# Kernel tuning notes

Hardware: AMD Instinct MI355X
Metric: run time of the kernel (lower is better)

## Reference

```python
import jax, jax.numpy as jnp
import numpy as np

N_VEH, N_PED = 16, 16
DV, DP = 40, 24            # vehicle / pedestrian slot obs dims
N = N_VEH + N_PED          # 32 agents
E, H = 128, 4              # embed_dim, num_heads
DH = E // H                # head_dim = 32
B = 4096
OBS = N_VEH * DV + N_PED * DP + N  # 1056


def setup_inputs() -> dict:
    key = jax.random.key(0)
    ks = jax.random.split(key, 12)
    s = lambda fan_in: 1.0 / np.sqrt(fan_in)
    inp = {
        "global_obs": jax.random.uniform(ks[0], (B, OBS), dtype=jnp.float32),
        # per-type projectors (stored as (in, out) so x @ W + b)
        "Wv": jax.random.uniform(ks[1], (DV, E), jnp.float32, -s(DV), s(DV)),
        "bv": jax.random.uniform(ks[2], (E,), jnp.float32, -s(DV), s(DV)),
        "Wp": jax.random.uniform(ks[3], (DP, E), jnp.float32, -s(DP), s(DP)),
        "bp": jax.random.uniform(ks[4], (E,), jnp.float32, -s(DP), s(DP)),
        # GAT layer 0 / 1: w (E, H*DH), a_src / a_dst (H, DH)
        "w0": jax.random.normal(ks[5], (E, H * DH), jnp.float32) * s(E),
        "asrc0": jax.random.normal(ks[6], (H, DH), jnp.float32) * s(DH),
        "adst0": jax.random.normal(ks[7], (H, DH), jnp.float32) * s(DH),
        "w1": jax.random.normal(ks[8], (E, H * DH), jnp.float32) * s(E),
        "asrc1": jax.random.normal(ks[9], (H, DH), jnp.float32) * s(DH),
        "adst1": jax.random.normal(ks[10], (H, DH), jnp.float32) * s(DH),
    }
    return inp


def _gat(x, alive, w, a_src, a_dst):
    # x: (B,N,E), alive: (B,N) in {0,1}
    b, n, _ = x.shape
    h = (x @ w).reshape(b, n, H, DH)                       # (B,N,H,DH)
    alpha_src = jnp.einsum("bnhd,hd->bnh", h, a_src)       # (B,N,H)
    alpha_dst = jnp.einsum("bnhd,hd->bnh", h, a_dst)
    e = alpha_src[:, :, None, :] + alpha_dst[:, None, :, :]  # (B,Ni,Nj,H)
    e = jnp.where(e > 0, e, 0.2 * e)                       # LeakyReLU(0.2)
    key_mask = alive[:, None, :, None] >= 0.5              # mask over j
    e = jnp.where(key_mask, e, -jnp.inf)
    attn = jax.nn.softmax(e, axis=2)                       # softmax over keys j
    attn = jnp.nan_to_num(attn)
    out = jnp.einsum("bijh,bjhd->bihd", attn, h)           # weighted aggregate
    return out.reshape(b, n, H * DH)                       # concat heads


def reference(global_obs, Wv, bv, Wp, bp, w0, asrc0, adst0, w1, asrc1, adst1):
    b = global_obs.shape[0]
    veh = global_obs[:, : N_VEH * DV].reshape(b, N_VEH, DV)
    ped = global_obs[:, N_VEH * DV : N_VEH * DV + N_PED * DP].reshape(b, N_PED, DP)
    alive_raw = global_obs[:, -N:]
    tokens = jnp.concatenate([veh @ Wv + bv, ped @ Wp + bp], axis=1)  # (B,N,E)
    alive = (alive_raw >= 0.5).astype(jnp.float32)
    all_dead = jnp.sum(alive, axis=1, keepdims=True) < 0.5
    alive = jnp.where(all_dead, jnp.ones_like(alive), alive)
    x = tokens
    for (w, a_s, a_d) in ((w0, asrc0, adst0), (w1, asrc1, adst1)):
        x = jax.nn.elu(_gat(x, alive, w, a_s, a_d))
    aw = alive[:, :, None]
    pooled = jnp.sum(x * aw, axis=1) / jnp.clip(jnp.sum(aw, axis=1), 1.0)
    return pooled
```

## Files before the change

kernel.cpp:

```cpp
#include <hip/hip_runtime.h>


#define NTOK 32
#define EMB  128
#define NH   4
#define OBSL 1056
#define XSTR 136
#define WSTR 72

typedef __attribute__((ext_vector_type(8))) short  short8;
typedef __attribute__((ext_vector_type(4))) float  floatx4;

__device__ __forceinline__ short f2bf(float f) {
  union { float f; unsigned u; } v; v.f = f;
  unsigned r = (v.u + 0x7fffu + ((v.u >> 16) & 1u)) >> 16;
  return (short)(unsigned short)r;
}
__device__ __forceinline__ float elu1(float v) { return v > 0.f ? v : __expf(v) - 1.f; }

__device__ __forceinline__ floatx4 mfma16(short8 a, short8 b, floatx4 c) {
  return __builtin_amdgcn_mfma_f32_16x16x32_bf16(a, b, c, 0, 0, 0);
}

__device__ __forceinline__ void stage_w_half(short* sw, const float* gw, int half, int tid) {
  const int e   = tid & 127;
  const int kk0 = (tid >> 7) * 32;
  const float* src = gw + (size_t)(half * 64 + kk0) * EMB + e;
  #pragma unroll
  for (int kk = 0; kk < 32; kk += 2) {
    float v0 = src[(size_t)kk * EMB];
    float v1 = src[(size_t)(kk + 1) * EMB];
    unsigned pk = (unsigned)(unsigned short)f2bf(v0) | ((unsigned)(unsigned short)f2bf(v1) << 16);
    *(unsigned*)&sw[e * WSTR + kk0 + kk] = pk;
  }
}

__global__ __launch_bounds__(256, 2) void gnn_fused(
    const float* __restrict__ obs,
    const float* __restrict__ Wv, const float* __restrict__ bv,
    const float* __restrict__ Wp, const float* __restrict__ bp,
    const float* __restrict__ w0, const float* __restrict__ as0, const float* __restrict__ ad0,
    const float* __restrict__ w1, const float* __restrict__ as1, const float* __restrict__ ad1,
    float* __restrict__ out)
{
  __shared__ __align__(16) short s_w[EMB * WSTR];
  __shared__ __align__(16) short s_xh[EMB * XSTR];
  __shared__ __align__(16) float s_alpha[2 * NH * 128];
  __shared__ __align__(16) float s_alive[128];
  __shared__ float s_inv[4];

  const int tid  = threadIdx.x;
  const int lane = tid & 63;
  const int wv   = tid >> 6;
  const int col  = lane & 15;
  const int quad = lane >> 4;
  const int b    = blockIdx.x * 4 + wv;

  const float* orow = obs + (size_t)b * OBSL;
  short* xbase = &s_xh[(wv * NTOK) * XSTR];
  const short8  z8 = {0,0,0,0,0,0,0,0};
  const floatx4 fz = {0.f,0.f,0.f,0.f};

  #pragma unroll
  for (int it = 0; it < 4; ++it) {
    int c = it * 64 + lane;
    *(short8*)&xbase[(c >> 3) * XSTR + (c & 7) * 8] = z8;
  }
  {
    float araw = (lane < NTOK) ? orow[1024 + lane] : 0.f;
    bool alv = (lane < NTOK) && (araw >= 0.5f);
    unsigned long long m = __ballot(alv);
    int cnt = __popcll(m);
    float flag = alv ? 1.f : 0.f;
    if (cnt == 0) { flag = (lane < NTOK) ? 1.f : 0.f; cnt = NTOK; }
    if (lane < NTOK) s_alive[wv * NTOK + lane] = flag;
    if (lane == 0) s_inv[wv] = 1.f / (float)cnt;
  }
  for (int idx = lane; idx < 1024; idx += 64) {
    float v = orow[idx];
    int r, k;
    if (idx < 640) { r = idx / 40; k = idx % 40; }
    else { int t2 = idx - 640; r = 16 + t2 / 24; k = 40 + t2 % 24; }
    xbase[r * XSTR + k] = f2bf(v);
  }
  {
    const int e = tid & 127;
    const int k0 = (tid >> 7) * 32;
    #pragma unroll
    for (int kk = 0; kk < 32; kk += 2) {
      int k = k0 + kk;
      float v0 = (k < 40) ? Wv[(size_t)k * EMB + e] : Wp[(size_t)(k - 40) * EMB + e];
      float v1 = (k + 1 < 40) ? Wv[(size_t)(k + 1) * EMB + e] : Wp[(size_t)(k + 1 - 40) * EMB + e];
      unsigned pk = (unsigned)(unsigned short)f2bf(v0) | ((unsigned)(unsigned short)f2bf(v1) << 16);
      *(unsigned*)&s_w[e * WSTR + k] = pk;
    }
  }
  __syncthreads();

  {
    short8 Aem[2][2];
    #pragma unroll
    for (int mtT = 0; mtT < 2; ++mtT)
      #pragma unroll
      for (int kt = 0; kt < 2; ++kt)
        Aem[mtT][kt] = *(const short8*)&s_xh[(wv * NTOK + mtT * 16 + col) * XSTR + kt * 32 + quad * 8];
    #pragma unroll
    for (int nt = 0; nt < 8; ++nt) {
      short8 B0 = *(const short8*)&s_w[(nt * 16 + col) * WSTR + quad * 8];
      short8 B1 = *(const short8*)&s_w[(nt * 16 + col) * WSTR + 32 + quad * 8];
      float bvv = bv[nt * 16 + col];
      float bpv = bp[nt * 16 + col];
      #pragma unroll
      for (int mtT = 0; mtT < 2; ++mtT) {
        floatx4 acc = fz;
        acc = mfma16(Aem[mtT][0], B0, acc);
        acc = mfma16(Aem[mtT][1], B1, acc);
        float bias = mtT ? bpv : bvv;
        #pragma unroll
        for (int r = 0; r < 4; ++r)
          s_xh[(wv * NTOK + mtT * 16 + quad * 4 + r) * XSTR + nt * 16 + col] = f2bf(acc[r] + bias);
      }
    }
  }

  const float* const gws[2] = {w0, w1};
  const float* const gass[2] = {as0, as1};
  const float* const gads[2] = {ad0, ad1};

  for (int L = 0; L < 2; ++L) {
    const float* gw  = gws[L];
    const float* gas = gass[L];
    const float* gad = gads[L];

    short8 Bx[4][2];
    #pragma unroll
    for (int kB = 0; kB < 4; ++kB)
      #pragma unroll
      for (int nt = 0; nt < 2; ++nt)
        Bx[kB][nt] = *(const short8*)&s_xh[(wv * NTOK + nt * 16 + col) * XSTR + kB * 32 + quad * 8];
    __syncthreads();
    stage_w_half(s_w, gw, 0, tid);
    __syncthreads();

    floatx4 acc[8][2];
    #pragma unroll
    for (int mt = 0; mt < 8; ++mt) { acc[mt][0] = fz; acc[mt][1] = fz; }
    #pragma unroll
    for (int mt = 0; mt < 8; ++mt) {
      short8 A0 = *(const short8*)&s_w[(mt * 16 + col) * WSTR + quad * 8];
      short8 A1 = *(const short8*)&s_w[(mt * 16 + col) * WSTR + 32 + quad * 8];
      #pragma unroll
      for (int nt = 0; nt < 2; ++nt) {
        acc[mt][nt] = mfma16(A0, Bx[0][nt], acc[mt][nt]);
        acc[mt][nt] = mfma16(A1, Bx[1][nt], acc[mt][nt]);
      }
    }
    __syncthreads();
    stage_w_half(s_w, gw, 1, tid);
    __syncthreads();
    #pragma unroll
    for (int mt = 0; mt < 8; ++mt) {
      short8 A0 = *(const short8*)&s_w[(mt * 16 + col) * WSTR + quad * 8];
      short8 A1 = *(const short8*)&s_w[(mt * 16 + col) * WSTR + 32 + quad * 8];
      #pragma unroll
      for (int nt = 0; nt < 2; ++nt) {
        acc[mt][nt] = mfma16(A0, Bx[2][nt], acc[mt][nt]);
        acc[mt][nt] = mfma16(A1, Bx[3][nt], acc[mt][nt]);
      }
    }

    float psrc[NH][2], pdst[NH][2];
    #pragma unroll
    for (int hh = 0; hh < NH; ++hh) { psrc[hh][0]=0.f; psrc[hh][1]=0.f; pdst[hh][0]=0.f; pdst[hh][1]=0.f; }
    #pragma unroll
    for (int mt = 0; mt < 8; ++mt) {
      const int hh = mt >> 1;
      float4 cs = *(const float4*)&gas[mt * 16 + quad * 4];
      float4 cd = *(const float4*)&gad[mt * 16 + quad * 4];
      #pragma unroll
      for (int nt = 0; nt < 2; ++nt) {
        floatx4 a = acc[mt][nt];
        psrc[hh][nt] += a[0]*cs.x + a[1]*cs.y + a[2]*cs.z + a[3]*cs.w;
        pdst[hh][nt] += a[0]*cd.x + a[1]*cd.y + a[2]*cd.z + a[3]*cd.w;
        #pragma unroll
        for (int r = 0; r < 4; ++r)
          s_xh[(mt * 16 + quad * 4 + r) * XSTR + wv * NTOK + nt * 16 + col] = f2bf(a[r]);
      }
    }
    #pragma unroll
    for (int hh = 0; hh < NH; ++hh)
      #pragma unroll
      for (int nt = 0; nt < 2; ++nt) {
        float vs = psrc[hh][nt], vd = pdst[hh][nt];
        vs += __shfl_xor(vs, 16); vs += __shfl_xor(vs, 32);
        vd += __shfl_xor(vd, 16); vd += __shfl_xor(vd, 32);
        if (quad == 0) {
          s_alpha[hh * 128 + wv * NTOK + nt * 16 + col] = vs;
          s_alpha[512 + hh * 128 + wv * NTOK + nt * 16 + col] = vd;
        }
      }

    float alv8[8];
    #pragma unroll
    for (int j = 0; j < 8; ++j) alv8[j] = s_alive[wv * NTOK + quad * 8 + j];
    short8 pfrag[NH][2];
    #pragma unroll
    for (int hh = 0; hh < NH; ++hh) {
      float ad8[8];
      #pragma unroll
      for (int j = 0; j < 8; ++j) ad8[j] = s_alpha[512 + hh * 128 + wv * NTOK + quad * 8 + j];
      #pragma unroll
      for (int ii = 0; ii < 2; ++ii) {
        float ai = s_alpha[hh * 128 + wv * NTOK + ii * 16 + col];
        float ev[8]; float mx = -1e30f;
        #pragma unroll
        for (int j = 0; j < 8; ++j) {
          float e = ai + ad8[j];
          e = e > 0.f ? e : 0.2f * e;
          e = (alv8[j] >= 0.5f) ? e : -1e30f;
          ev[j] = e; mx = fmaxf(mx, e);
        }
        mx = fmaxf(mx, __shfl_xor(mx, 16));
        mx = fmaxf(mx, __shfl_xor(mx, 32));
        float sum = 0.f;
        #pragma unroll
        for (int j = 0; j < 8; ++j) { float p = __expf(ev[j] - mx); ev[j] = p; sum += p; }
        sum += __shfl_xor(sum, 16);
        sum += __shfl_xor(sum, 32);
        float inv = 1.f / sum;
        short8 pf;
        #pragma unroll
        for (int j = 0; j < 8; ++j) pf[j] = f2bf(ev[j] * inv);
        pfrag[hh][ii] = pf;
      }
    }

    short8 Ah[NH][2];
    #pragma unroll
    for (int hh = 0; hh < NH; ++hh)
      #pragma unroll
      for (int mtE = 0; mtE < 2; ++mtE)
        Ah[hh][mtE] = *(const short8*)&s_xh[(hh * 32 + mtE * 16 + col) * XSTR + wv * NTOK + quad * 8];
    __syncthreads();

    floatx4 po[NH][2][2];
    #pragma unroll
    for (int hh = 0; hh < NH; ++hh)
      #pragma unroll
      for (int mtE = 0; mtE < 2; ++mtE) { po[hh][mtE][0] = fz; po[hh][mtE][1] = fz; }
    #pragma unroll
    for (int hh = 0; hh < NH; ++hh)
      #pragma unroll
      for (int mtE = 0; mtE < 2; ++mtE)
        #pragma unroll
        for (int nt = 0; nt < 2; ++nt)
          po[hh][mtE][nt] = mfma16(Ah[hh][mtE], pfrag[hh][nt], po[hh][mtE][nt]);

    if (L == 0) {
      #pragma unroll
      for (int hh = 0; hh < NH; ++hh)
        #pragma unroll
        for (int mtE = 0; mtE < 2; ++mtE)
          #pragma unroll
          for (int nt = 0; nt < 2; ++nt)
            #pragma unroll
            for (int r = 0; r < 4; ++r) {
              float v = elu1(po[hh][mtE][nt][r]);
              s_xh[(wv * NTOK + nt * 16 + col) * XSTR + hh * 32 + mtE * 16 + quad * 4 + r] = f2bf(v);
            }
    } else {
      float alvI0 = s_alive[wv * NTOK + col];
      float alvI1 = s_alive[wv * NTOK + 16 + col];
      float invc = s_inv[wv];
      #pragma unroll
      for (int hh = 0; hh < NH; ++hh)
        #pragma unroll
        for (int mtE = 0; mtE < 2; ++mtE)
          #pragma unroll
          for (int r = 0; r < 4; ++r) {
            float s = elu1(po[hh][mtE][0][r]) * alvI0 + elu1(po[hh][mtE][1][r]) * alvI1;
            s += __shfl_xor(s, 1); s += __shfl_xor(s, 2);
            s += __shfl_xor(s, 4); s += __shfl_xor(s, 8);
            if (col == 0)
              s_alpha[wv * 128 + hh * 32 + mtE * 16 + quad * 4 + r] = s;
          }
      float r0 = s_alpha[wv * 128 + lane];
      float r1 = s_alpha[wv * 128 + 64 + lane];
      out[(size_t)b * EMB + lane]      = r0 * invc;
      out[(size_t)b * EMB + 64 + lane] = r1 * invc;
    }
  }
}

extern "C" void kernel_launch(void* const* d_in, const int* in_sizes, int n_in,
                              void* d_out, int out_size, void* d_ws, size_t ws_size,
                              hipStream_t stream) {
  const float* obs = (const float*)d_in[0];
  const float* Wv  = (const float*)d_in[1];
  const float* bv  = (const float*)d_in[2];
  const float* Wp  = (const float*)d_in[3];
  const float* bp  = (const float*)d_in[4];
  const float* w0  = (const float*)d_in[5];
  const float* as0 = (const float*)d_in[6];
  const float* ad0 = (const float*)d_in[7];
  const float* w1  = (const float*)d_in[8];
  const float* as1 = (const float*)d_in[9];
  const float* ad1 = (const float*)d_in[10];
  float* out = (float*)d_out;

  int Bn = in_sizes[0] / OBSL;
  dim3 grid(Bn / 4), block(256);
  gnn_fused<<<grid, block, 0, stream>>>(obs, Wv, bv, Wp, bp, w0, as0, ad0, w1, as1, ad1, out);
}
```

Baseline: 146.7 us.

## Pre-convert weights to bf16 in a prep kernel and read them from global memory

A separate prep kernel now converts and transposes all weight matrices to bf16 in workspace once per call. The main kernel reads MFMA fragments straight from global/L2 instead of staging each block's weights in LDS, which removes the weight shared buffer and several barriers. It also moves alive flags and attention logits to registers via shuffles, uses hardware packed bf16 conversion, and raises the occupancy hint to 4 blocks. The trade-offs are an extra kernel launch and more repeated L2 reads of the weights.

```diff
diff --git a/kernel.cpp b/kernel.cpp
--- a/kernel.cpp
+++ b/kernel.cpp
@@ -3,51 +3,53 @@
 
 #define NTOK 32
 #define EMB  128
-#define NH   4
 #define OBSL 1056
 #define XSTR 136
-#define WSTR 72
 
 typedef __attribute__((ext_vector_type(8))) short  short8;
 typedef __attribute__((ext_vector_type(4))) float  floatx4;
+typedef __attribute__((ext_vector_type(2))) unsigned uint2v;
 
 __device__ __forceinline__ short f2bf(float f) {
   union { float f; unsigned u; } v; v.f = f;
   unsigned r = (v.u + 0x7fffu + ((v.u >> 16) & 1u)) >> 16;
   return (short)(unsigned short)r;
 }
+__device__ __forceinline__ unsigned pk2(float a, float b) {
+  unsigned r; asm("v_cvt_pk_bf16_f32 %0, %1, %2" : "=v"(r) : "v"(a), "v"(b)); return r;
+}
 __device__ __forceinline__ float elu1(float v) { return v > 0.f ? v : __expf(v) - 1.f; }
-
 __device__ __forceinline__ floatx4 mfma16(short8 a, short8 b, floatx4 c) {
   return __builtin_amdgcn_mfma_f32_16x16x32_bf16(a, b, c, 0, 0, 0);
 }
 
-__device__ __forceinline__ void stage_w_half(short* sw, const float* gw, int half, int tid) {
-  const int e   = tid & 127;
-  const int kk0 = (tid >> 7) * 32;
-  const float* src = gw + (size_t)(half * 64 + kk0) * EMB + e;
-  #pragma unroll
-  for (int kk = 0; kk < 32; kk += 2) {
-    float v0 = src[(size_t)kk * EMB];
-    float v1 = src[(size_t)(kk + 1) * EMB];
-    unsigned pk = (unsigned)(unsigned short)f2bf(v0) | ((unsigned)(unsigned short)f2bf(v1) << 16);
-    *(unsigned*)&sw[e * WSTR + kk0 + kk] = pk;
-  }
-}
-
-__global__ __launch_bounds__(256, 2) void gnn_fused(
+__global__ void prep_weights(const float* __restrict__ Wv, const float* __restrict__ Wp,
+                             const float* __restrict__ w0, const float* __restrict__ w1,
+                             short* __restrict__ ws) {
+  int idx = blockIdx.x * 256 + threadIdx.x;
+  if (idx < 8192) {
+    int e = idx >> 6, k = idx & 63;
+    float v = (k < 40) ? Wv[(size_t)k * EMB + e] : Wp[(size_t)(k - 40) * EMB + e];
+    ws[idx] = f2bf(v);
+  } else if (idx < 24576) {
+    int t = idx - 8192; int e = t >> 7, k = t & 127;
+    ws[idx] = f2bf(w0[(size_t)k * EMB + e]);
+  } else {
+    int t = idx - 24576; int e = t >> 7, k = t & 127;
+    ws[idx] = f2bf(w1[(size_t)k * EMB + e]);
+  }
+}
+
+__global__ __launch_bounds__(256, 4) void gnn_fused(
     const float* __restrict__ obs,
-    const float* __restrict__ Wv, const float* __restrict__ bv,
-    const float* __restrict__ Wp, const float* __restrict__ bp,
-    const float* __restrict__ w0, const float* __restrict__ as0, const float* __restrict__ ad0,
-    const float* __restrict__ w1, const float* __restrict__ as1, const float* __restrict__ ad1,
+    const float* __restrict__ bv, const float* __restrict__ bp,
+    const float* __restrict__ as0, const float* __restrict__ ad0,
+    const float* __restrict__ as1, const float* __restrict__ ad1,
+    const short* __restrict__ wsb,
     float* __restrict__ out)
 {
-  __shared__ __align__(16) short s_w[EMB * WSTR];
   __shared__ __align__(16) short s_xh[EMB * XSTR];
-  __shared__ __align__(16) float s_alpha[2 * NH * 128];
-  __shared__ __align__(16) float s_alive[128];
-  __shared__ float s_inv[4];
+  __shared__ float s_pool[4 * EMB];
 
   const int tid  = threadIdx.x;
   const int lane = tid & 63;
@@ -61,235 +63,205 @@
   const short8  z8 = {0,0,0,0,0,0,0,0};
   const floatx4 fz = {0.f,0.f,0.f,0.f};
 
-  #pragma unroll
-  for (int it = 0; it < 4; ++it) {
-    int c = it * 64 + lane;
-    *(short8*)&xbase[(c >> 3) * XSTR + (c & 7) * 8] = z8;
-  }
+  float flag; float invc;
   {
     float araw = (lane < NTOK) ? orow[1024 + lane] : 0.f;
     bool alv = (lane < NTOK) && (araw >= 0.5f);
     unsigned long long m = __ballot(alv);
     int cnt = __popcll(m);
-    float flag = alv ? 1.f : 0.f;
+    flag = alv ? 1.f : 0.f;
     if (cnt == 0) { flag = (lane < NTOK) ? 1.f : 0.f; cnt = NTOK; }
-    if (lane < NTOK) s_alive[wv * NTOK + lane] = flag;
-    if (lane == 0) s_inv[wv] = 1.f / (float)cnt;
-  }
-  for (int idx = lane; idx < 1024; idx += 64) {
+    invc = 1.f / (float)cnt;
+  }
+  float alv8[8];
+  #pragma unroll
+  for (int jj = 0; jj < 8; ++jj) alv8[jj] = __shfl(flag, quad * 8 + jj);
+  const float alvI0 = __shfl(flag, col);
+  const float alvI1 = __shfl(flag, 16 + col);
+
+  #pragma unroll
+  for (int it = 0; it < 4; ++it) {
+    int c = it * 64 + lane;
+    *(short8*)&xbase[(c >> 3) * XSTR + (c & 7) * 8] = z8;
+  }
+  #pragma unroll
+  for (int it = 0; it < 16; ++it) {
+    int idx = it * 64 + lane;
     float v = orow[idx];
     int r, k;
     if (idx < 640) { r = idx / 40; k = idx % 40; }
     else { int t2 = idx - 640; r = 16 + t2 / 24; k = 40 + t2 % 24; }
     xbase[r * XSTR + k] = f2bf(v);
   }
+
   {
-    const int e = tid & 127;
-    const int k0 = (tid >> 7) * 32;
-    #pragma unroll
-    for (int kk = 0; kk < 32; kk += 2) {
-      int k = k0 + kk;
-      float v0 = (k < 40) ? Wv[(size_t)k * EMB + e] : Wp[(size_t)(k - 40) * EMB + e];
-      float v1 = (k + 1 < 40) ? Wv[(size_t)(k + 1) * EMB + e] : Wp[(size_t)(k + 1 - 40) * EMB + e];
-      unsigned pk = (unsigned)(unsigned short)f2bf(v0) | ((unsigned)(unsigned short)f2bf(v1) << 16);
-      *(unsigned*)&s_w[e * WSTR + k] = pk;
+    short8 Bxin[2][2];
+    #pragma unroll
+    for (int nt = 0; nt < 2; ++nt)
+      #pragma unroll
+      for (int kt = 0; kt < 2; ++kt)
+        Bxin[nt][kt] = *(const short8*)&xbase[(nt * 16 + col) * XSTR + kt * 32 + quad * 8];
+    const short* embT = wsb;
+    #pragma unroll
+    for (int mtE = 0; mtE < 8; ++mtE) {
+      short8 A0 = *(const short8*)&embT[(mtE * 16 + col) * 64 + quad * 8];
+      short8 A1 = *(const short8*)&embT[(mtE * 16 + col) * 64 + 32 + quad * 8];
+      float4 bv4 = *(const float4*)&bv[mtE * 16 + quad * 4];
+      float4 bp4 = *(const float4*)&bp[mtE * 16 + quad * 4];
+      #pragma unroll
+      for (int nt = 0; nt < 2; ++nt) {
+        floatx4 acc = fz;
+        acc = mfma16(A0, Bxin[nt][0], acc);
+        acc = mfma16(A1, Bxin[nt][1], acc);
+        float4 bb = nt ? bp4 : bv4;
+        uint2v u; u.x = pk2(acc[0] + bb.x, acc[1] + bb.y); u.y = pk2(acc[2] + bb.z, acc[3] + bb.w);
+        *(uint2v*)&xbase[(nt * 16 + col) * XSTR + mtE * 16 + quad * 4] = u;
+      }
     }
   }
-  __syncthreads();
-
-  {
-    short8 Aem[2][2];
-    #pragma unroll
-    for (int mtT = 0; mtT < 2; ++mtT)
-      #pragma unroll
-      for (int kt = 0; kt < 2; ++kt)
-        Aem[mtT][kt] = *(const short8*)&s_xh[(wv * NTOK + mtT * 16 + col) * XSTR + kt * 32 + quad * 8];
-    #pragma unroll
-    for (int nt = 0; nt < 8; ++nt) {
-      short8 B0 = *(const short8*)&s_w[(nt * 16 + col) * WSTR + quad * 8];
-      short8 B1 = *(const short8*)&s_w[(nt * 16 + col) * WSTR + 32 + quad * 8];
-      float bvv = bv[nt * 16 + col];
-      float bpv = bp[nt * 16 + col];
-      #pragma unroll
-      for (int mtT = 0; mtT < 2; ++mtT) {
-        floatx4 acc = fz;
-        acc = mfma16(Aem[mtT][0], B0, acc);
-        acc = mfma16(Aem[mtT][1], B1, acc);
-        float bias = mtT ? bpv : bvv;
-        #pragma unroll
-        for (int r = 0; r < 4; ++r)
-          s_xh[(wv * NTOK + mtT * 16 + quad * 4 + r) * XSTR + nt * 16 + col] = f2bf(acc[r] + bias);
+
+  for (int L = 0; L < 2; ++L) {
+    const short* wT  = wsb + 8192 + L * 16384;
+    const float* gas = L ? as1 : as0;
+    const float* gad = L ? ad1 : ad0;
+
+    short8 Bx[4][2];
+    #pragma unroll
+    for (int kt = 0; kt < 4; ++kt)
+      #pragma unroll
+      for (int nt = 0; nt < 2; ++nt)
+        Bx[kt][nt] = *(const short8*)&xbase[(nt * 16 + col) * XSTR + kt * 32 + quad * 8];
+    __syncthreads();
+
+    float psrc[4][2], pdst[4][2];
+    #pragma unroll
+    for (int hh = 0; hh < 4; ++hh) { psrc[hh][0]=0.f; psrc[hh][1]=0.f; pdst[hh][0]=0.f; pdst[hh][1]=0.f; }
+    #pragma unroll
+    for (int g = 0; g < 2; ++g) {
+      floatx4 acc[4][2];
+      #pragma unroll
+      for (int mi = 0; mi < 4; ++mi) { acc[mi][0] = fz; acc[mi][1] = fz; }
+      #pragma unroll
+      for (int mi = 0; mi < 4; ++mi) {
+        const int mt = g * 4 + mi;
+        const short* wrow = &wT[(mt * 16 + col) * 128 + quad * 8];
+        short8 A0 = *(const short8*)&wrow[0];
+        short8 A1 = *(const short8*)&wrow[32];
+        short8 A2 = *(const short8*)&wrow[64];
+        short8 A3 = *(const short8*)&wrow[96];
+        #pragma unroll
+        for (int nt = 0; nt < 2; ++nt) {
+          acc[mi][nt] = mfma16(A0, Bx[0][nt], acc[mi][nt]);
+          acc[mi][nt] = mfma16(A1, Bx[1][nt], acc[mi][nt]);
+          acc[mi][nt] = mfma16(A2, Bx[2][nt], acc[mi][nt]);
+          acc[mi][nt] = mfma16(A3, Bx[3][nt], acc[mi][nt]);
+        }
+      }
+      #pragma unroll
+      for (int mi = 0; mi < 4; ++mi) {
+        const int mt = g * 4 + mi;
+        const int hh = mt >> 1;
+        float4 cs = *(const float4*)&gas[mt * 16 + quad * 4];
+        float4 cd = *(const float4*)&gad[mt * 16 + quad * 4];
+        #pragma unroll
+        for (int nt = 0; nt < 2; ++nt) {
+          floatx4 a = acc[mi][nt];
+          psrc[hh][nt] += a[0]*cs.x + a[1]*cs.y + a[2]*cs.z + a[3]*cs.w;
+          pdst[hh][nt] += a[0]*cd.x + a[1]*cd.y + a[2]*cd.z + a[3]*cd.w;
+          unsigned u01 = pk2(a[0], a[1]);
+          unsigned u23 = pk2(a[2], a[3]);
+          unsigned short* hrow = (unsigned short*)&s_xh[(mt * 16 + quad * 4) * XSTR + wv * NTOK + nt * 16 + col];
+          hrow[0]        = (unsigned short)u01;
+          hrow[XSTR]     = (unsigned short)(u01 >> 16);
+          hrow[2 * XSTR] = (unsigned short)u23;
+          hrow[3 * XSTR] = (unsigned short)(u23 >> 16);
+        }
       }
     }
-  }
-
-  const float* const gws[2] = {w0, w1};
-  const float* const gass[2] = {as0, as1};
-  const float* const gads[2] = {ad0, ad1};
-
-  for (int L = 0; L < 2; ++L) {
-    const float* gw  = gws[L];
-    const float* gas = gass[L];
-    const float* gad = gads[L];
-
-    short8 Bx[4][2];
-    #pragma unroll
-    for (int kB = 0; kB < 4; ++kB)
-      #pragma unroll
-      for (int nt = 0; nt < 2; ++nt)
-        Bx[kB][nt] = *(const short8*)&s_xh[(wv * NTOK + nt * 16 + col) * XSTR + kB * 32 + quad * 8];
-    __syncthreads();
-    stage_w_half(s_w, gw, 0, tid);
-    __syncthreads();
-
-    floatx4 acc[8][2];
-    #pragma unroll
-    for (int mt = 0; mt < 8; ++mt) { acc[mt][0] = fz; acc[mt][1] = fz; }
-    #pragma unroll
-    for (int mt = 0; mt < 8; ++mt) {
-      short8 A0 = *(const short8*)&s_w[(mt * 16 + col) * WSTR + quad * 8];
-      short8 A1 = *(const short8*)&s_w[(mt * 16 + col) * WSTR + 32 + quad * 8];
+
+    #pragma unroll
+    for (int hh = 0; hh < 4; ++hh)
       #pragma unroll
       for (int nt = 0; nt < 2; ++nt) {
-        acc[mt][nt] = mfma16(A0, Bx[0][nt], acc[mt][nt]);
-        acc[mt][nt] = mfma16(A1, Bx[1][nt], acc[mt][nt]);
-      }
-    }
-    __syncthreads();
-    stage_w_half(s_w, gw, 1, tid);
-    __syncthreads();
-    #pragma unroll
-    for (int mt = 0; mt < 8; ++mt) {
-      short8 A0 = *(const short8*)&s_w[(mt * 16 + col) * WSTR + quad * 8];
-      short8 A1 = *(const short8*)&s_w[(mt * 16 + col) * WSTR + 32 + quad * 8];
-      #pragma unroll
-      for (int nt = 0; nt < 2; ++nt) {
-        acc[mt][nt] = mfma16(A0, Bx[2][nt], acc[mt][nt]);
-        acc[mt][nt] = mfma16(A1, Bx[3][nt], acc[mt][nt]);
-      }
-    }
-
-    float psrc[NH][2], pdst[NH][2];
-    #pragma unroll
-    for (int hh = 0; hh < NH; ++hh) { psrc[hh][0]=0.f; psrc[hh][1]=0.f; pdst[hh][0]=0.f; pdst[hh][1]=0.f; }
-    #pragma unroll
-    for (int mt = 0; mt < 8; ++mt) {
-      const int hh = mt >> 1;
-      float4 cs = *(const float4*)&gas[mt * 16 + quad * 4];
-      float4 cd = *(const float4*)&gad[mt * 16 + quad * 4];
-      #pragma unroll
-      for (int nt = 0; nt < 2; ++nt) {
-        floatx4 a = acc[mt][nt];
-        psrc[hh][nt] += a[0]*cs.x + a[1]*cs.y + a[2]*cs.z + a[3]*cs.w;
-        pdst[hh][nt] += a[0]*cd.x + a[1]*cd.y + a[2]*cd.z + a[3]*cd.w;
-        #pragma unroll
-        for (int r = 0; r < 4; ++r)
-          s_xh[(mt * 16 + quad * 4 + r) * XSTR + wv * NTOK + nt * 16 + col] = f2bf(a[r]);
-      }
-    }
-    #pragma unroll
-    for (int hh = 0; hh < NH; ++hh)
-      #pragma unroll
-      for (int nt = 0; nt < 2; ++nt) {
-        float vs = psrc[hh][nt], vd = pdst[hh][nt];
-        vs += __shfl_xor(vs, 16); vs += __shfl_xor(vs, 32);
-        vd += __shfl_xor(vd, 16); vd += __shfl_xor(vd, 32);
-        if (quad == 0) {
-          s_alpha[hh * 128 + wv * NTOK + nt * 16 + col] = vs;
-          s_alpha[512 + hh * 128 + wv * NTOK + nt * 16 + col] = vd;
-        }
-      }
-
-    float alv8[8];
-    #pragma unroll
-    for (int j = 0; j < 8; ++j) alv8[j] = s_alive[wv * NTOK + quad * 8 + j];
-    short8 pfrag[NH][2];
-    #pragma unroll
-    for (int hh = 0; hh < NH; ++hh) {
+        float vs = psrc[hh][nt]; vs += __shfl_xor(vs, 16); vs += __shfl_xor(vs, 32); psrc[hh][nt] = vs;
+        float vd = pdst[hh][nt]; vd += __shfl_xor(vd, 16); vd += __shfl_xor(vd, 32); pdst[hh][nt] = vd;
+      }
+
+    short8 pf[4][2];
+    #pragma unroll
+    for (int hh = 0; hh < 4; ++hh) {
+      float vsel = (quad >> 1) ? pdst[hh][1] : pdst[hh][0];
       float ad8[8];
       #pragma unroll
-      for (int j = 0; j < 8; ++j) ad8[j] = s_alpha[512 + hh * 128 + wv * NTOK + quad * 8 + j];
+      for (int jj = 0; jj < 8; ++jj)
+        ad8[jj] = __shfl(vsel, ((quad >> 1) << 5) + ((quad & 1) << 3) + jj);
       #pragma unroll
       for (int ii = 0; ii < 2; ++ii) {
-        float ai = s_alpha[hh * 128 + wv * NTOK + ii * 16 + col];
-        float ev[8]; float mx = -1e30f;
-        #pragma unroll
-        for (int j = 0; j < 8; ++j) {
-          float e = ai + ad8[j];
+        float ai = psrc[hh][ii];
+        float ev[8]; float mx = -3e38f;
+        #pragma unroll
+        for (int jj = 0; jj < 8; ++jj) {
+          float e = ai + ad8[jj];
           e = e > 0.f ? e : 0.2f * e;
-          e = (alv8[j] >= 0.5f) ? e : -1e30f;
-          ev[j] = e; mx = fmaxf(mx, e);
+          e = (alv8[jj] >= 0.5f) ? e : -1e30f;
+          ev[jj] = e; mx = fmaxf(mx, e);
         }
         mx = fmaxf(mx, __shfl_xor(mx, 16));
         mx = fmaxf(mx, __shfl_xor(mx, 32));
         float sum = 0.f;
         #pragma unroll
-        for (int j = 0; j < 8; ++j) { float p = __expf(ev[j] - mx); ev[j] = p; sum += p; }
+        for (int jj = 0; jj < 8; ++jj) { float p = __expf(ev[jj] - mx); ev[jj] = p; sum += p; }
         sum += __shfl_xor(sum, 16);
         sum += __shfl_xor(sum, 32);
         float inv = 1.f / sum;
-        short8 pf;
-        #pragma unroll
-        for (int j = 0; j < 8; ++j) pf[j] = f2bf(ev[j] * inv);
-        pfrag[hh][ii] = pf;
+        union { unsigned u4[4]; short8 s; } pu;
+        #pragma unroll
+        for (int p = 0; p < 4; ++p) pu.u4[p] = pk2(ev[2*p] * inv, ev[2*p+1] * inv);
+        pf[hh][ii] = pu.s;
       }
     }
 
-    short8 Ah[NH][2];
-    #pragma unroll
-    for (int hh = 0; hh < NH; ++hh)
+    short8 Ah[4][2];
+    #pragma unroll
+    for (int hh = 0; hh < 4; ++hh)
       #pragma unroll
       for (int mtE = 0; mtE < 2; ++mtE)
         Ah[hh][mtE] = *(const short8*)&s_xh[(hh * 32 + mtE * 16 + col) * XSTR + wv * NTOK + quad * 8];
-    __syncthreads();
-
-    floatx4 po[NH][2][2];
-    #pragma unroll
-    for (int hh = 0; hh < NH; ++hh)
-      #pragma unroll
-      for (int mtE = 0; mtE < 2; ++mtE) { po[hh][mtE][0] = fz; po[hh][mtE][1] = fz; }
-    #pragma unroll
-    for (int hh = 0; hh < NH; ++hh)
-      #pragma unroll
-      for (int mtE = 0; mtE < 2; ++mtE)
-        #pragma unroll
-        for (int nt = 0; nt < 2; ++nt)
-          po[hh][mtE][nt] = mfma16(Ah[hh][mtE], pfrag[hh][nt], po[hh][mtE][nt]);
-
-    if (L == 0) {
-      #pragma unroll
-      for (int hh = 0; hh < NH; ++hh)
-        #pragma unroll
-        for (int mtE = 0; mtE < 2; ++mtE)
+    if (L == 0) __syncthreads();
+
+    #pragma unroll
+    for (int hh = 0; hh < 4; ++hh)
+      #pragma unroll
+      for (int mtE = 0; mtE < 2; ++mtE) {
+        floatx4 po[2];
+        #pragma unroll
+        for (int nt = 0; nt < 2; ++nt) {
+          po[nt] = mfma16(Ah[hh][mtE], pf[hh][nt], fz);
+        }
+        if (L == 0) {
           #pragma unroll
-          for (int nt = 0; nt < 2; ++nt)
-            #pragma unroll
-            for (int r = 0; r < 4; ++r) {
-              float v = elu1(po[hh][mtE][nt][r]);
-              s_xh[(wv * NTOK + nt * 16 + col) * XSTR + hh * 32 + mtE * 16 + quad * 4 + r] = f2bf(v);
-            }
-    } else {
-      float alvI0 = s_alive[wv * NTOK + col];
-      float alvI1 = s_alive[wv * NTOK + 16 + col];
-      float invc = s_inv[wv];
-      #pragma unroll
-      for (int hh = 0; hh < NH; ++hh)
-        #pragma unroll
-        for (int mtE = 0; mtE < 2; ++mtE)
+          for (int nt = 0; nt < 2; ++nt) {
+            uint2v u;
+            u.x = pk2(elu1(po[nt][0]), elu1(po[nt][1]));
+            u.y = pk2(elu1(po[nt][2]), elu1(po[nt][3]));
+            *(uint2v*)&xbase[(nt * 16 + col) * XSTR + hh * 32 + mtE * 16 + quad * 4] = u;
+          }
+        } else {
           #pragma unroll
           for (int r = 0; r < 4; ++r) {
-            float s = elu1(po[hh][mtE][0][r]) * alvI0 + elu1(po[hh][mtE][1][r]) * alvI1;
+            float s = elu1(po[0][r]) * alvI0 + elu1(po[1][r]) * alvI1;
             s += __shfl_xor(s, 1); s += __shfl_xor(s, 2);
             s += __shfl_xor(s, 4); s += __shfl_xor(s, 8);
-            if (col == 0)
-              s_alpha[wv * 128 + hh * 32 + mtE * 16 + quad * 4 + r] = s;
+            if (col == 0) s_pool[wv * EMB + hh * 32 + mtE * 16 + quad * 4 + r] = s;
           }
-      float r0 = s_alpha[wv * 128 + lane];
-      float r1 = s_alpha[wv * 128 + 64 + lane];
-      out[(size_t)b * EMB + lane]      = r0 * invc;
-      out[(size_t)b * EMB + 64 + lane] = r1 * invc;
-    }
-  }
+        }
+      }
+  }
+
+  float r0 = s_pool[wv * EMB + lane];
+  float r1 = s_pool[wv * EMB + 64 + lane];
+  out[(size_t)b * EMB + lane]      = r0 * invc;
+  out[(size_t)b * EMB + 64 + lane] = r1 * invc;
 }
 
 extern "C" void kernel_launch(void* const* d_in, const int* in_sizes, int n_in,
@@ -307,8 +279,9 @@
   const float* as1 = (const float*)d_in[9];
   const float* ad1 = (const float*)d_in[10];
   float* out = (float*)d_out;
+  short* wsb = (short*)d_ws;
 
   int Bn = in_sizes[0] / OBSL;
-  dim3 grid(Bn / 4), block(256);
-  gnn_fused<<<grid, block, 0, stream>>>(obs, Wv, bv, Wp, bp, w0, as0, ad0, w1, as1, ad1, out);
-}
+  prep_weights<<<160, 256, 0, stream>>>(Wv, Wp, w0, w1, wsb);
+  gnn_fused<<<Bn / 4, 256, 0, stream>>>(obs, bv, bp, as0, ad0, as1, ad1, wsb, out);
+}
```

Result: faster. 139.1 us (-5.2%).
